# Performance work log

Hardware: AMD Instinct MI355X
Metric: run time of the kernel (lower is better)

## Reference

```python
import jax, jax.numpy as jnp
import numpy as np

N = 16384          # nodes
E_R = 524288       # radial edges (avg degree 32)
E_B = 32768        # bonded edges
N_TYPES = 20       # atom types
CS = 64            # scalar (0e) channels
CV = 32            # vector (1o) channels
EA = 16            # edge_attr_dim
EA_B = EA // 2     # bondedness embedding dim
EA_R = (EA + 1) // 2  # radial basis dim
CUTOFF = 1.5       # effective_radial_cutoff
L = 2              # n_layers
NORM = float(np.sqrt((E_R + E_B) / N))  # ~sqrt(avg degree) message normalization


def setup_inputs() -> dict:
    key = jax.random.key(0)
    ks = jax.random.split(key, 32)
    def rn(i, shape, scale=1.0):
        return jax.random.normal(ks[i], shape, dtype=jnp.float32) * scale
    s_e = 1.0 / np.sqrt(EA)
    inp = {}
    inp["pos"] = rn(0, (N, 3))
    inp["c_noise"] = rn(1, (1,))
    inp["atom_types"] = jax.random.randint(ks[2], (N,), 0, N_TYPES)
    inp["radial_edge_index"] = jax.random.randint(ks[3], (2, E_R), 0, N)
    inp["bonded_edge_index"] = jax.random.randint(ks[4], (2, E_B), 0, N)
    # learned parameters
    inp["atom_tab"] = rn(5, (N_TYPES, CS))
    inp["bond_tab"] = rn(6, (2, EA_B))
    inp["ns0_w"] = rn(7, (CS,), 0.1)
    inp["We0"] = rn(8, (EA, CS), s_e)
    inp["We1"] = rn(9, (EA, CS), s_e)
    inp["Wself0"] = rn(10, (CS, CS), 1.0 / np.sqrt(CS))
    inp["Ws0"] = rn(11, (CS, CS), 1.0 / np.sqrt(CS))
    inp["Wv0"] = rn(12, (CS, CV), 1.0 / np.sqrt(CS))
    inp["ns_w"] = rn(13, (L, CS + CV), 0.1)
    inp["We_ss"] = rn(14, (L, EA, CS), s_e)
    inp["We_vs"] = rn(15, (L, EA, CV), s_e)
    inp["We_sv"] = rn(16, (L, EA, CS), s_e)
    inp["We_vv"] = rn(17, (L, EA, CV), s_e)
    inp["We_vx"] = rn(18, (L, EA, CV), s_e)
    inp["Wmix_s"] = rn(19, (L, CS + CV, CS), 1.0 / np.sqrt(CS + CV))
    inp["Wmix_v"] = rn(20, (L, CS + 2 * CV, CV), 1.0 / np.sqrt(CS + 2 * CV))
    inp["Wself_s"] = rn(21, (L, CS, CS), 1.0 / np.sqrt(CS))
    inp["Wself_v"] = rn(22, (L, CV, CV), 1.0 / np.sqrt(CV))
    inp["skip_w"] = rn(23, (L, 2 * (CS + CV)), 0.1)
    inp["skip_b"] = rn(24, (L, 2 * (CS + CV)), 0.1)
    inp["w_out"] = rn(25, (CV,), 1.0 / np.sqrt(CV))
    inp["gain"] = jnp.asarray(0.5, dtype=jnp.float32)
    return inp


def _radial_basis(d):
    # e3nn soft_one_hot_linspace, basis='gaussian', cutoff=True
    centers = jnp.linspace(0.0, CUTOFF, EA_R + 2)[1:-1]
    step = centers[1] - centers[0]
    diff = (d[:, None] - centers[None, :]) / step
    return jnp.exp(-diff * diff) * 1.12


def reference(pos, c_noise, atom_tab, bond_tab, ns0_w, We0, We1, Wself0, Ws0, Wv0,
              ns_w, We_ss, We_vs, We_sv, We_vv, We_vx, Wmix_s, Wmix_v, Wself_s, Wself_v,
              skip_w, skip_b, w_out, gain, atom_types, radial_edge_index, bonded_edge_index):
    edge_index = jnp.concatenate([radial_edge_index, bonded_edge_index], axis=1)
    bond_mask = jnp.concatenate([jnp.zeros((E_R,), jnp.int32), jnp.ones((E_B,), jnp.int32)])
    src, dst = edge_index[0], edge_index[1]
    edge_vec = pos[src] - pos[dst]                      # [E,3]
    d = jnp.sqrt(jnp.sum(edge_vec * edge_vec, -1) + 1e-12)
    Y1 = jnp.sqrt(3.0) * edge_vec / d[:, None]          # l=1 SH, component norm; Y0 == 1
    edge_attr = jnp.concatenate([bond_tab[bond_mask], _radial_basis(d)], axis=-1)  # [E,EA]

    # atom embedding + initial noise-conditional scaling
    s = atom_tab[atom_types] * (1.0 + c_noise * ns0_w)  # [N,CS]

    # initial projector: scalar-input equivariant conv -> hidden irreps
    w0 = edge_attr @ We0
    w1 = edge_attr @ We1
    s_src = s[src]
    a_s = jax.ops.segment_sum(w0 * s_src, dst, num_segments=N) / NORM
    a_v = jax.ops.segment_sum((w1 * s_src)[:, :, None] * Y1[:, None, :], dst, num_segments=N) / NORM
    s_h = a_s @ Ws0 + s @ Wself0                        # [N,CS]
    v_h = jnp.einsum('nci,cd->ndi', a_v, Wv0)           # [N,CV,3]

    for l in range(L):
        # noise-conditional scaling (per-irrep-channel scalar scale)
        scale = 1.0 + c_noise * ns_w[l]
        ss = s_h * scale[:CS]
        vv = v_h * scale[CS:][None, :, None]
        ss_e = ss[src]
        vv_e = vv[src]
        # edge-attr-conditioned tensor-product weights
        w_ss = edge_attr @ We_ss[l]
        w_vs = edge_attr @ We_vs[l]
        w_sv = edge_attr @ We_sv[l]
        w_vv = edge_attr @ We_vv[l]
        w_vx = edge_attr @ We_vx[l]
        # CG tensor-product messages: 0x0->0, 1x1->0 (dot), 0x1->1, 1x0->1, 1x1->1 (cross)
        vdot = jnp.einsum('eci,ei->ec', vv_e, Y1)
        m_s = jnp.concatenate([w_ss * ss_e, w_vs * vdot], axis=-1)          # [E,CS+CV]
        m_v = jnp.concatenate([
            (w_sv * ss_e)[:, :, None] * Y1[:, None, :],
            w_vv[:, :, None] * vv_e,
            w_vx[:, :, None] * jnp.cross(vv_e, Y1[:, None, :]),
        ], axis=1)                                                          # [E,CS+2CV,3]
        a_s = jax.ops.segment_sum(m_s, dst, num_segments=N) / NORM
        a_v = jax.ops.segment_sum(m_v, dst, num_segments=N) / NORM
        new_s = a_s @ Wmix_s[l] + ss @ Wself_s[l]
        new_v = jnp.einsum('nci,cd->ndi', a_v, Wmix_v[l]) + jnp.einsum('nci,cd->ndi', vv, Wself_v[l])
        # noise-conditional skip connection (gated residual)
        g = jax.nn.sigmoid(skip_b[l] + c_noise * skip_w[l])
        s_h = g[:CS] * s_h + g[CS:2 * CS] * new_s
        g_v = g[2 * CS:]
        v_h = g_v[:CV][None, :, None] * v_h + g_v[CV:][None, :, None] * new_v

    # output head: 1o vectors -> 3D displacement, times output gain
    return jnp.einsum('nci,c->ni', v_h, w_out) * gain
```

## Files before the change

### kernel.cpp

```cpp
#include <hip/hip_runtime.h>
#include <math.h>

#define NA 16384
#define ER 524288
#define EB 32768
#define ET 557056
#define INV_NORM 0.17149858514250882f
#define SQRT3 1.7320508075688772f
#define RB_STEP (1.5f/9.0f)
#define BINS 512
#define DMAX 2.5f
#define INV_H ((float)BINS / DMAX)
#define T0U (2 * BINS * 128)
#define TLU (2 * BINS * 256)

typedef unsigned int uint32;
typedef unsigned short ushort16;

__device__ __forceinline__ float sigmoidf_(float x) { return 1.f / (1.f + __expf(-x)); }

__device__ __forceinline__ ushort16 f2bf(float x) {
  uint32 u = __float_as_uint(x);
  u = u + 0x7FFFu + ((u >> 16) & 1u);
  return (ushort16)(u >> 16);
}
__device__ __forceinline__ uint32 packbf(float hi, float lo) {
  return ((uint32)f2bf(hi) << 16) | (uint32)f2bf(lo);
}
__device__ __forceinline__ float bfhi(uint32 u) { return __uint_as_float(u & 0xFFFF0000u); }
__device__ __forceinline__ float bflo(uint32 u) { return __uint_as_float(u << 16); }

__global__ void k_zero(int* __restrict__ count) {
  count[blockIdx.x * 256 + threadIdx.x] = 0;
}

__global__ void k_hist(const int* __restrict__ rad, const int* __restrict__ bon, int* __restrict__ count) {
  int e = blockIdx.x * 256 + threadIdx.x;
  int d = (e < ER) ? rad[ER + e] : bon[EB + (e - ER)];
  atomicAdd(&count[d], 1);
}

__global__ __launch_bounds__(1024) void k_scan_all(const int* __restrict__ count,
                                                   int* __restrict__ offsets,
                                                   int* __restrict__ cursor,
                                                   int* __restrict__ order) {
  __shared__ int ts[1024];
  __shared__ int hist[256];
  __shared__ int hcur[256];
  int t = threadIdx.x;
  if (t < 256) hist[t] = 0;
  int base = t * 16;
  int loc[16], cnts[16];
  int sum = 0;
#pragma unroll
  for (int i = 0; i < 16; ++i) { cnts[i] = count[base + i]; loc[i] = sum; sum += cnts[i]; }
  ts[t] = sum;
  __syncthreads();
#pragma unroll
  for (int i = 0; i < 16; ++i) atomicAdd(&hist[cnts[i] < 255 ? cnts[i] : 255], 1);
  for (int off = 1; off < 1024; off <<= 1) {
    int x = (t >= off) ? ts[t - off] : 0;
    __syncthreads();
    ts[t] += x;
    __syncthreads();
  }
  int excl = ts[t] - sum;
#pragma unroll
  for (int i = 0; i < 16; ++i) {
    int v = excl + loc[i];
    offsets[base + i] = v;
    cursor[base + i] = v;
  }
  if (t == 1023) offsets[NA] = excl + sum;
  __syncthreads();
  if (t == 0) {
    int run = 0;
    for (int d = 255; d >= 0; --d) { hcur[d] = run; run += hist[d]; }
  }
  __syncthreads();
#pragma unroll
  for (int i = 0; i < 16; ++i) {
    int d = cnts[i] < 255 ? cnts[i] : 255;
    int p = atomicAdd(&hcur[d], 1);
    order[p] = base + i;
  }
}

__global__ void k_fill_pre(const int* __restrict__ rad, const int* __restrict__ bon,
                           int* __restrict__ cursor, const float* __restrict__ pos,
                           float* __restrict__ rec8) {
  int e = blockIdx.x * 256 + threadIdx.x;
  int src, dst, v;
  if (e < ER) { src = rad[e]; dst = rad[ER + e]; v = 0; }
  else        { src = bon[e - ER]; dst = bon[EB + e - ER]; v = 1; }
  float dx = pos[src * 3] - pos[dst * 3];
  float dy = pos[src * 3 + 1] - pos[dst * 3 + 1];
  float dz = pos[src * 3 + 2] - pos[dst * 3 + 2];
  float dist = sqrtf(dx * dx + dy * dy + dz * dz + 1e-12f);
  float inv = 1.f / dist;
  float fq = fminf(dist * INV_H, BINS - 1.001f);
  int q = (int)fq;
  float frac = fq - (float)q;
  int qoffL = (v * BINS + q) << 8;
  int slot = atomicAdd(&cursor[dst], 1);
  float* rp = rec8 + (size_t)slot * 8;
  *(float4*)rp = make_float4(__int_as_float(src), SQRT3 * dx * inv, SQRT3 * dy * inv, SQRT3 * dz * inv);
  rp[4] = frac;
  rp[5] = __int_as_float(qoffL);
}

__global__ void k_build(const float* __restrict__ We0, const float* __restrict__ We1,
                        const float* __restrict__ We_ss, const float* __restrict__ We_vs,
                        const float* __restrict__ We_sv, const float* __restrict__ We_vv,
                        const float* __restrict__ We_vx, const float* __restrict__ bond_tab,
                        uint32* __restrict__ T0, uint32* __restrict__ TL) {
  int q = blockIdx.x, t = blockIdx.y, v = blockIdx.z, c = threadIdx.x;
  float d0 = q * (DMAX / BINS), d1 = (q + 1) * (DMAX / BINS);
  float rb0[8], rb1[8];
#pragma unroll
  for (int k = 0; k < 8; ++k) {
    float f0 = (d0 - (k + 1) * RB_STEP) * (1.f / RB_STEP);
    float f1 = (d1 - (k + 1) * RB_STEP) * (1.f / RB_STEP);
    rb0[k] = 1.12f * __expf(-f0 * f0);
    rb1[k] = 1.12f * __expf(-f1 * f1);
  }
  if (t == 0) {
    float ba = 0, bb = 0, a0 = 0, a1 = 0, b0 = 0, b1 = 0;
#pragma unroll
    for (int k = 0; k < 8; ++k) {
      float bt = bond_tab[v * 8 + k];
      float av_lo = We0[k * 64 + c], av_hi = We0[(8 + k) * 64 + c];
      float bv_lo = We1[k * 64 + c], bv_hi = We1[(8 + k) * 64 + c];
      ba += bt * av_lo; bb += bt * bv_lo;
      a0 += rb0[k] * av_hi; a1 += rb1[k] * av_hi;
      b0 += rb0[k] * bv_hi; b1 += rb1[k] * bv_hi;
    }
    uint32* o = T0 + (((size_t)v * BINS + q) << 7) + c * 2;
    o[0] = packbf(ba + a0, a1 - a0);
    o[1] = packbf(bb + b0, b1 - b0);
  } else {
    int l = t - 1;
    const float* Wss = We_ss + l * 1024;
    const float* Wsv = We_sv + l * 1024;
    const float* WA = (c < 32) ? (We_vs + l * 512) : (We_vx + l * 512);
    const float* WB = (c < 32) ? (We_vv + l * 512) : nullptr;
    int cu = c & 31;
    float sa = 0, sb = 0, s0 = 0, s1 = 0, t0 = 0, t1 = 0;
    float ua = 0, ub = 0, u0 = 0, u1 = 0, w0 = 0, w1 = 0;
#pragma unroll
    for (int k = 0; k < 8; ++k) {
      float bt = bond_tab[v * 8 + k];
      float ss_lo = Wss[k * 64 + c], ss_hi = Wss[(8 + k) * 64 + c];
      float sv_lo = Wsv[k * 64 + c], sv_hi = Wsv[(8 + k) * 64 + c];
      sa += bt * ss_lo; sb += bt * sv_lo;
      s0 += rb0[k] * ss_hi; s1 += rb1[k] * ss_hi;
      t0 += rb0[k] * sv_hi; t1 += rb1[k] * sv_hi;
      float a_lo = WA[k * 32 + cu], a_hi = WA[(8 + k) * 32 + cu];
      ua += bt * a_lo;
      u0 += rb0[k] * a_hi; u1 += rb1[k] * a_hi;
      if (WB) {
        float b_lo = WB[k * 32 + cu], b_hi = WB[(8 + k) * 32 + cu];
        ub += bt * b_lo;
        w0 += rb0[k] * b_hi; w1 += rb1[k] * b_hi;
      }
    }
    uint32* o = TL + (size_t)l * TLU + (((size_t)v * BINS + q) << 8) + c * 4;
    o[0] = packbf(sa + s0, s1 - s0);
    o[1] = packbf(sb + t0, t1 - t0);
    o[2] = packbf(ua + u0, u1 - u0);
    o[3] = WB ? packbf(ub + w0, w1 - w0) : 0u;
  }
}

__global__ void k_embed(const float* __restrict__ atom_tab, const int* __restrict__ types,
                        const float* __restrict__ ns0_w, const float* __restrict__ cnoise,
                        float* __restrict__ s_feat, ushort16* __restrict__ s_bf) {
  int tid = blockIdx.x * 256 + threadIdx.x;
  int n = tid >> 6, c = tid & 63;
  float cn = cnoise[0];
  float v = atom_tab[types[n] * 64 + c] * (1.f + cn * ns0_w[c]);
  s_feat[tid] = v;
  s_bf[tid] = f2bf(v);
}

#define AISSUE(S, eidx) { \
    const float* rp_ = rec8 + (size_t)(eidx) * 8; \
    float4 ra_ = *(const float4*)rp_; float2 rb_ = *(const float2*)(rp_ + 4); \
    S##_f = rb_.x; S##_y0 = ra_.y; S##_y1 = ra_.z; S##_y2 = ra_.w; \
    S##_t = *(const uint2*)(T0c + ((((unsigned)__float_as_int(rb_.y)) << 1) + laneT)); \
    S##_s = *(const ushort16*)(SBc + ((((unsigned)__float_as_int(ra_.x)) << 7) + laneS)); \
  }
#define ACOMP(S) { \
    float w0_ = fmaf(S##_f, bflo(S##_t.x), bfhi(S##_t.x)); \
    float w1_ = fmaf(S##_f, bflo(S##_t.y), bfhi(S##_t.y)); \
    float sv_ = __uint_as_float((uint32)S##_s << 16); \
    acc += w0_ * sv_; \
    float t_ = w1_ * sv_; \
    a0 += t_ * S##_y0; a1 += t_ * S##_y1; a2 += t_ * S##_y2; \
  }

__global__ __launch_bounds__(256, 8) void k_agg0(
    const int* __restrict__ offsets, const int* __restrict__ order,
    const float* __restrict__ rec8,
    const uint32* __restrict__ T0, const ushort16* __restrict__ s_bf,
    float* __restrict__ a_s, float* __restrict__ a_v) {
  int lane = threadIdx.x & 63;
  int n = __builtin_amdgcn_readfirstlane(order[blockIdx.x * 4 + (threadIdx.x >> 6)]);
  const char* T0c = (const char*)T0;
  const char* SBc = (const char*)s_bf;
  unsigned laneT = (unsigned)lane * 8u;
  unsigned laneS = (unsigned)lane * 2u;
  float acc = 0, a0 = 0, a1 = 0, a2 = 0;
  int beg = __builtin_amdgcn_readfirstlane(offsets[n]);
  int end = __builtin_amdgcn_readfirstlane(offsets[n + 1]);
  float S0_f, S0_y0, S0_y1, S0_y2; uint2 S0_t; ushort16 S0_s;
  float S1_f, S1_y0, S1_y1, S1_y2; uint2 S1_t; ushort16 S1_s;
  float S2_f, S2_y0, S2_y1, S2_y2; uint2 S2_t; ushort16 S2_s;
  if (beg < end) {
    int last = end - 1;
    AISSUE(S0, beg);
    AISSUE(S1, (beg + 1 < end) ? beg + 1 : last);
    AISSUE(S2, (beg + 2 < end) ? beg + 2 : last);
    int i = beg;
    while (i + 3 <= end) {
      ACOMP(S0); AISSUE(S0, (i + 3 < end) ? i + 3 : last);
      ACOMP(S1); AISSUE(S1, (i + 4 < end) ? i + 4 : last);
      ACOMP(S2); AISSUE(S2, (i + 5 < end) ? i + 5 : last);
      i += 3;
    }
    int rem = end - i;
    if (rem >= 1) ACOMP(S0);
    if (rem >= 2) ACOMP(S1);
  }
  a_s[n * 64 + lane] = acc * INV_NORM;
  *(float4*)(a_v + ((size_t)n << 8) + (lane << 2)) =
      make_float4(a0 * INV_NORM, a1 * INV_NORM, a2 * INV_NORM, 0.f);
}

#define LISSUE(S, eidx) { \
    const float* rp_ = rec8 + (size_t)(eidx) * 8; \
    float4 ra_ = *(const float4*)rp_; float2 rb_ = *(const float2*)(rp_ + 4); \
    S##_f = rb_.x; S##_y0 = ra_.y; S##_y1 = ra_.z; S##_y2 = ra_.w; \
    S##_t = *(const uint4*)(TLc + ((((unsigned)__float_as_int(rb_.y)) << 2) + laneT)); \
    unsigned sb_ = (unsigned)__float_as_int(ra_.x); \
    S##_s = *(const ushort16*)(SHc + ((sb_ << 7) + laneS)); \
    S##_v = *(const uint2*)(VHc + ((sb_ << 8) + laneV)); \
  }
#define LCOMP(S) { \
    float wS_  = fmaf(S##_f, bflo(S##_t.x), bfhi(S##_t.x)); \
    float wSV_ = fmaf(S##_f, bflo(S##_t.y), bfhi(S##_t.y)); \
    float wA_  = fmaf(S##_f, bflo(S##_t.z), bfhi(S##_t.z)); \
    float wB_  = fmaf(S##_f, bflo(S##_t.w), bfhi(S##_t.w)); \
    float ss_ = __uint_as_float((uint32)S##_s << 16); \
    float vx_ = bfhi(S##_v.x), vy_ = bflo(S##_v.x), vz_ = bfhi(S##_v.y); \
    ms += wS_ * ss_; \
    float t_ = wSV_ * ss_; \
    av0 += t_ * S##_y0; av1 += t_ * S##_y1; av2 += t_ * S##_y2; \
    float vdot_ = vx_ * S##_y0 + vy_ * S##_y1 + vz_ * S##_y2; \
    ms2 += wA_ * vdot_; \
    float cx_ = vy_ * S##_y2 - vz_ * S##_y1; \
    float cy_ = vz_ * S##_y0 - vx_ * S##_y2; \
    float cz_ = vx_ * S##_y1 - vy_ * S##_y0; \
    float wM_ = low ? wB_ : wA_; \
    b0 += wM_ * (low ? vx_ : cx_); \
    b1 += wM_ * (low ? vy_ : cy_); \
    b2 += wM_ * (low ? vz_ : cz_); \
  }

__global__ __launch_bounds__(256, 8) void k_agg_layer(
    const float* __restrict__ cnoise, const float* __restrict__ nsw,
    const int* __restrict__ offsets, const int* __restrict__ order,
    const float* __restrict__ rec8,
    const uint32* __restrict__ TL, const ushort16* __restrict__ sh_bf,
    const uint32* __restrict__ vh_bf,
    float* __restrict__ a_s, float* __restrict__ a_v) {
  int lane = threadIdx.x & 63;
  int n = __builtin_amdgcn_readfirstlane(order[blockIdx.x * 4 + (threadIdx.x >> 6)]);
  int vc = lane & 31;
  bool low = lane < 32;
  const char* TLc = (const char*)TL;
  const char* SHc = (const char*)sh_bf;
  const char* VHc = (const char*)vh_bf;
  unsigned laneT = (unsigned)lane * 16u;
  unsigned laneS = (unsigned)lane * 2u;
  unsigned laneV = (unsigned)vc * 8u;
  float cn = cnoise[0];
  float scale_s = 1.f + cn * nsw[lane];
  float scale_v = 1.f + cn * nsw[64 + vc];
  float ms = 0, av0 = 0, av1 = 0, av2 = 0, ms2 = 0, b0 = 0, b1 = 0, b2 = 0;
  int beg = __builtin_amdgcn_readfirstlane(offsets[n]);
  int end = __builtin_amdgcn_readfirstlane(offsets[n + 1]);
  float S0_f, S0_y0, S0_y1, S0_y2; uint4 S0_t; ushort16 S0_s; uint2 S0_v;
  float S1_f, S1_y0, S1_y1, S1_y2; uint4 S1_t; ushort16 S1_s; uint2 S1_v;
  float S2_f, S2_y0, S2_y1, S2_y2; uint4 S2_t; ushort16 S2_s; uint2 S2_v;
  if (beg < end) {
    int last = end - 1;
    LISSUE(S0, beg);
    LISSUE(S1, (beg + 1 < end) ? beg + 1 : last);
    LISSUE(S2, (beg + 2 < end) ? beg + 2 : last);
    int i = beg;
    while (i + 3 <= end) {
      LCOMP(S0); LISSUE(S0, (i + 3 < end) ? i + 3 : last);
      LCOMP(S1); LISSUE(S1, (i + 4 < end) ? i + 4 : last);
      LCOMP(S2); LISSUE(S2, (i + 5 < end) ? i + 5 : last);
      i += 3;
    }
    int rem = end - i;
    if (rem >= 1) LCOMP(S0);
    if (rem >= 2) LCOMP(S1);
  }
  float fs = scale_s * INV_NORM;
  float fv = scale_v * INV_NORM;
  a_s[n * 96 + lane] = ms * fs;
  float* avn = a_v + ((size_t)n << 9);
  *(float4*)(avn + (lane << 2)) = make_float4(av0 * fs, av1 * fs, av2 * fs, 0.f);
  if (low) {
    a_s[n * 96 + 64 + vc] = ms2 * fv;
    *(float4*)(avn + ((64 + vc) << 2)) = make_float4(b0 * fv, b1 * fv, b2 * fv, 0.f);
  } else {
    *(float4*)(avn + ((96 + vc) << 2)) = make_float4(b0 * fv, b1 * fv, b2 * fv, 0.f);
  }
}

__global__ __launch_bounds__(256, 4) void k_init_s(
    const float* __restrict__ a_s, const float* __restrict__ s_feat,
    const float* __restrict__ Ws0, const float* __restrict__ Wself0,
    float* __restrict__ sh, ushort16* __restrict__ sh_bf) {
  __shared__ float W1[64 * 64];
  __shared__ float W2[64 * 64];
  __shared__ float La[8 * 64];
  __shared__ float Lf[8 * 64];
  int tid = threadIdx.x;
  for (int i = tid; i < 1024; i += 256) {
    ((float4*)W1)[i] = ((const float4*)Ws0)[i];
    ((float4*)W2)[i] = ((const float4*)Wself0)[i];
  }
  int base = blockIdx.x * 8;
  for (int i = tid; i < 512; i += 256) {
    La[i] = a_s[(size_t)base * 64 + i];
    Lf[i] = s_feat[(size_t)base * 64 + i];
  }
  __syncthreads();
  int d = tid & 63, g = tid >> 6;
  int n0 = base + g * 2;
  const float* A0 = La + g * 128;
  const float* A1 = A0 + 64;
  const float* F0 = Lf + g * 128;
  const float* F1 = F0 + 64;
  float a0 = 0, a1 = 0;
#pragma unroll 8
  for (int c = 0; c < 64; ++c) {
    float w1 = W1[c * 64 + d], w2 = W2[c * 64 + d];
    a0 += A0[c] * w1 + F0[c] * w2;
    a1 += A1[c] * w1 + F1[c] * w2;
  }
  sh[(size_t)n0 * 64 + d] = a0;
  sh[(size_t)(n0 + 1) * 64 + d] = a1;
  sh_bf[(size_t)n0 * 64 + d] = f2bf(a0);
  sh_bf[(size_t)(n0 + 1) * 64 + d] = f2bf(a1);
}

__global__ __launch_bounds__(256, 4) void k_init_v(
    const float* __restrict__ a_v, const float* __restrict__ Wv0,
    float* __restrict__ vh, uint32* __restrict__ vh_bf) {
  __shared__ float W[64 * 32];
  int tid = threadIdx.x;
  for (int i = tid; i < 512; i += 256) ((float4*)W)[i] = ((const float4*)Wv0)[i];
  __syncthreads();
  int d = tid & 31, g = tid >> 5;
  int n = blockIdx.x * 8 + g;
  const float4* av = (const float4*)(a_v + ((size_t)n << 8));
  float x = 0, y = 0, z = 0;
#pragma unroll 4
  for (int c = 0; c < 64; ++c) {
    float4 a = av[c];
    float w = W[c * 32 + d];
    x += a.x * w; y += a.y * w; z += a.z * w;
  }
  *(float4*)(vh + ((size_t)n << 7) + (d << 2)) = make_float4(x, y, z, 0.f);
  *(uint2*)(vh_bf + ((size_t)n << 6) + (d << 1)) = make_uint2(packbf(x, y), packbf(z, 0.f));
}

__global__ __launch_bounds__(256, 4) void k_mix_s(
    const float* __restrict__ a_s, const float* __restrict__ sh_in,
    const float* __restrict__ Wmix_s, const float* __restrict__ Wself_s,
    const float* __restrict__ nsw, const float* __restrict__ skw,
    const float* __restrict__ skb, const float* __restrict__ cnoise,
    float* __restrict__ sh_out, ushort16* __restrict__ sh_bf_out) {
  __shared__ float Wm[96 * 64];
  __shared__ float Wsf[64 * 64];
  __shared__ float La[8 * 96];
  int tid = threadIdx.x;
  float cn = cnoise[0];
  for (int i = tid; i < 96 * 16; i += 256) ((float4*)Wm)[i] = ((const float4*)Wmix_s)[i];
  for (int i = tid; i < 64 * 16; i += 256) {
    float4 wv = ((const float4*)Wself_s)[i];
    int c = i >> 4;
    float sc = 1.f + cn * nsw[c];
    wv.x *= sc; wv.y *= sc; wv.z *= sc; wv.w *= sc;
    ((float4*)Wsf)[i] = wv;
  }
  int base = blockIdx.x * 8;
  for (int i = tid; i < 8 * 96; i += 256) La[i] = a_s[(size_t)base * 96 + i];
  __syncthreads();
  int d = tid & 63, g = tid >> 6;
  int n0 = base + g * 2;
  const float* A0 = La + (g * 2) * 96;
  const float* A1 = A0 + 96;
  const float* s0p = sh_in + (size_t)n0 * 64;
  const float* s1p = s0p + 64;
  float acc0 = 0, acc1 = 0;
#pragma unroll 8
  for (int c = 0; c < 96; ++c) {
    float w = Wm[c * 64 + d];
    acc0 += A0[c] * w;
    acc1 += A1[c] * w;
  }
#pragma unroll 8
  for (int c = 0; c < 64; ++c) {
    float w = Wsf[c * 64 + d];
    acc0 += s0p[c] * w;
    acc1 += s1p[c] * w;
  }
  float g1 = sigmoidf_(skb[d] + cn * skw[d]);
  float g2 = sigmoidf_(skb[64 + d] + cn * skw[64 + d]);
  float o0 = g1 * s0p[d] + g2 * acc0;
  float o1 = g1 * s1p[d] + g2 * acc1;
  sh_out[(size_t)n0 * 64 + d] = o0;
  sh_out[(size_t)(n0 + 1) * 64 + d] = o1;
  sh_bf_out[(size_t)n0 * 64 + d] = f2bf(o0);
  sh_bf_out[(size_t)(n0 + 1) * 64 + d] = f2bf(o1);
}

__global__ __launch_bounds__(256, 4) void k_mix_v(
    const float* __restrict__ a_v, const float* __restrict__ vh_in,
    const float* __restrict__ Wmix_v, const float* __restrict__ Wself_v,
    const float* __restrict__ nsw, const float* __restrict__ skw,
    const float* __restrict__ skb, const float* __restrict__ cnoise,
    float* __restrict__ vh_out, uint32* __restrict__ vh_bf_out) {
  __shared__ float Wm[128 * 32];
  __shared__ float Wsf[32 * 32];
  int tid = threadIdx.x;
  float cn = cnoise[0];
  for (int i = tid; i < 128 * 8; i += 256) ((float4*)Wm)[i] = ((const float4*)Wmix_v)[i];
  for (int i = tid; i < 32 * 8; i += 256) {
    float4 wv = ((const float4*)Wself_v)[i];
    int c = i >> 3;
    float sc = 1.f + cn * nsw[64 + c];
    wv.x *= sc; wv.y *= sc; wv.z *= sc; wv.w *= sc;
    ((float4*)Wsf)[i] = wv;
  }
  __syncthreads();
  int d = tid & 31, g = tid >> 5;
  int n = blockIdx.x * 8 + g;
  const float4* av = (const float4*)(a_v + ((size_t)n << 9));
  const float4* vr = (const float4*)(vh_in + ((size_t)n << 7));
  float x = 0, y = 0, z = 0;
#pragma unroll 4
  for (int c = 0; c < 128; ++c) {
    float4 a = av[c];
    float w = Wm[c * 32 + d];
    x += a.x * w; y += a.y * w; z += a.z * w;
  }
#pragma unroll 4
  for (int c = 0; c < 32; ++c) {
    float4 vv = vr[c];
    float w = Wsf[c * 32 + d];
    x += vv.x * w; y += vv.y * w; z += vv.z * w;
  }
  float g3 = sigmoidf_(skb[128 + d] + cn * skw[128 + d]);
  float g4 = sigmoidf_(skb[160 + d] + cn * skw[160 + d]);
  float4 vi = vr[d];
  float ox = g3 * vi.x + g4 * x;
  float oy = g3 * vi.y + g4 * y;
  float oz = g3 * vi.z + g4 * z;
  *(float4*)(vh_out + ((size_t)n << 7) + (d << 2)) = make_float4(ox, oy, oz, 0.f);
  *(uint2*)(vh_bf_out + ((size_t)n << 6) + (d << 1)) = make_uint2(packbf(ox, oy), packbf(oz, 0.f));
}

__global__ void k_out(const float* __restrict__ vh, const float* __restrict__ w_out,
                      const float* __restrict__ gain, float* __restrict__ out) {
  int tid = blockIdx.x * 256 + threadIdx.x;
  int n = tid / 3, i = tid - n * 3;
  float acc = 0;
  for (int c = 0; c < 32; ++c) acc += vh[((size_t)n << 7) + c * 4 + i] * w_out[c];
  out[tid] = acc * gain[0];
}

extern "C" void kernel_launch(void* const* d_in, const int* in_sizes, int n_in,
                              void* d_out, int out_size, void* d_ws, size_t ws_size,
                              hipStream_t stream) {
  (void)in_sizes; (void)n_in; (void)out_size; (void)ws_size;
  const float* pos     = (const float*)d_in[0];
  const float* cn      = (const float*)d_in[1];
  const int*   types   = (const int*)d_in[2];
  const int*   rad     = (const int*)d_in[3];
  const int*   bon     = (const int*)d_in[4];
  const float* atom_tab= (const float*)d_in[5];
  const float* bond_tab= (const float*)d_in[6];
  const float* ns0_w   = (const float*)d_in[7];
  const float* We0     = (const float*)d_in[8];
  const float* We1     = (const float*)d_in[9];
  const float* Wself0  = (const float*)d_in[10];
  const float* Ws0     = (const float*)d_in[11];
  const float* Wv0     = (const float*)d_in[12];
  const float* ns_w    = (const float*)d_in[13];
  const float* We_ss   = (const float*)d_in[14];
  const float* We_vs   = (const float*)d_in[15];
  const float* We_sv   = (const float*)d_in[16];
  const float* We_vv   = (const float*)d_in[17];
  const float* We_vx   = (const float*)d_in[18];
  const float* Wmix_s  = (const float*)d_in[19];
  const float* Wmix_v  = (const float*)d_in[20];
  const float* Wself_s = (const float*)d_in[21];
  const float* Wself_v = (const float*)d_in[22];
  const float* skip_w  = (const float*)d_in[23];
  const float* skip_b  = (const float*)d_in[24];
  const float* w_out   = (const float*)d_in[25];
  const float* gain    = (const float*)d_in[26];

  char* ws = (char*)d_ws;
  size_t o = 0;
  auto alloc = [&](size_t bytes) -> void* {
    void* p = ws + o;
    o += (bytes + 255) & ~(size_t)255;
    return p;
  };
  float* s_feat  = (float*)alloc((size_t)NA * 64 * 4);
  ushort16* s_bf = (ushort16*)alloc((size_t)NA * 64 * 2);
  float* a_s     = (float*)alloc((size_t)NA * 96 * 4);
  float* a_v     = (float*)alloc((size_t)NA * 512 * 4);
  float* sh0     = (float*)alloc((size_t)NA * 64 * 4);
  float* sh1     = (float*)alloc((size_t)NA * 64 * 4);
  ushort16* shbf0= (ushort16*)alloc((size_t)NA * 64 * 2);
  ushort16* shbf1= (ushort16*)alloc((size_t)NA * 64 * 2);
  float* vh0     = (float*)alloc((size_t)NA * 128 * 4);
  float* vh1     = (float*)alloc((size_t)NA * 128 * 4);
  uint32* vhbf0  = (uint32*)alloc((size_t)NA * 64 * 4);
  uint32* vhbf1  = (uint32*)alloc((size_t)NA * 64 * 4);
  int* count     = (int*)alloc((size_t)NA * 4);
  int* offsets   = (int*)alloc((size_t)(NA + 1) * 4);
  int* cursor    = (int*)alloc((size_t)NA * 4);
  int* order     = (int*)alloc((size_t)NA * 4);
  float* rec8    = (float*)alloc((size_t)ET * 32);
  uint32* T0     = (uint32*)alloc((size_t)T0U * 4);
  uint32* TL     = (uint32*)alloc((size_t)2 * TLU * 4);
  float* shb[2]  = {sh0, sh1};
  ushort16* shbf[2] = {shbf0, shbf1};
  float* vhb[2]  = {vh0, vh1};
  uint32* vhbf[2]= {vhbf0, vhbf1};

  k_zero<<<NA / 256, 256, 0, stream>>>(count);
  k_hist<<<ET / 256, 256, 0, stream>>>(rad, bon, count);
  k_scan_all<<<1, 1024, 0, stream>>>(count, offsets, cursor, order);
  k_fill_pre<<<ET / 256, 256, 0, stream>>>(rad, bon, cursor, pos, rec8);
  k_build<<<dim3(BINS, 3, 2), 64, 0, stream>>>(We0, We1, We_ss, We_vs, We_sv, We_vv, We_vx,
                                               bond_tab, T0, TL);

  k_embed<<<NA * 64 / 256, 256, 0, stream>>>(atom_tab, types, ns0_w, cn, s_feat, s_bf);
  k_agg0<<<NA / 4, 256, 0, stream>>>(offsets, order, rec8, T0, s_bf, a_s, a_v);
  k_init_s<<<NA / 8, 256, 0, stream>>>(a_s, s_feat, Ws0, Wself0, shb[0], shbf[0]);
  k_init_v<<<NA / 8, 256, 0, stream>>>(a_v, Wv0, vhb[0], vhbf[0]);

  for (int l = 0; l < 2; ++l) {
    int bin = l & 1, bout = 1 - bin;
    k_agg_layer<<<NA / 4, 256, 0, stream>>>(
        cn, ns_w + l * 96, offsets, order, rec8, TL + (size_t)l * TLU, shbf[bin], vhbf[bin], a_s, a_v);
    k_mix_s<<<NA / 8, 256, 0, stream>>>(
        a_s, shb[bin], Wmix_s + l * 96 * 64, Wself_s + l * 64 * 64,
        ns_w + l * 96, skip_w + l * 192, skip_b + l * 192, cn, shb[bout], shbf[bout]);
    k_mix_v<<<NA / 8, 256, 0, stream>>>(
        a_v, vhb[bin], Wmix_v + l * 128 * 32, Wself_v + l * 32 * 32,
        ns_w + l * 96, skip_w + l * 192, skip_b + l * 192, cn, vhb[bout], vhbf[bout]);
  }
  k_out<<<NA * 3 / 256, 256, 0, stream>>>(vhb[0], w_out, gain, (float*)d_out);
}
```

Before: 479.1 us.

## Skip dead scalar path in last layer and fuse init/mix/output kernels

The final layer's scalar aggregation and scalar mix are dropped, because only the vector features reach the output head. The scalar and vector init kernels are merged into one launch, as are the scalar and vector mix kernels, by splitting on block index. The output projection is folded into the last vector mix with a wave shuffle reduction, and the zeroing kernel becomes a memset. This cuts launch count and skips unneeded compute and stores, at the cost of larger fused kernels whose LDS footprint may limit occupancy.

```diff
diff --git a/kernel.cpp b/kernel.cpp
--- a/kernel.cpp
+++ b/kernel.cpp
@@ -29,10 +29,6 @@
 }
 __device__ __forceinline__ float bfhi(uint32 u) { return __uint_as_float(u & 0xFFFF0000u); }
 __device__ __forceinline__ float bflo(uint32 u) { return __uint_as_float(u << 16); }
-
-__global__ void k_zero(int* __restrict__ count) {
-  count[blockIdx.x * 256 + threadIdx.x] = 0;
-}
 
 __global__ void k_hist(const int* __restrict__ rad, const int* __restrict__ bon, int* __restrict__ count) {
   int e = blockIdx.x * 256 + threadIdx.x;
@@ -266,6 +262,22 @@
     b1 += wM_ * (low ? vy_ : cy_); \
     b2 += wM_ * (low ? vz_ : cz_); \
   }
+#define LCOMP_NS(S) { \
+    float wSV_ = fmaf(S##_f, bflo(S##_t.y), bfhi(S##_t.y)); \
+    float wA_  = fmaf(S##_f, bflo(S##_t.z), bfhi(S##_t.z)); \
+    float wB_  = fmaf(S##_f, bflo(S##_t.w), bfhi(S##_t.w)); \
+    float ss_ = __uint_as_float((uint32)S##_s << 16); \
+    float vx_ = bfhi(S##_v.x), vy_ = bflo(S##_v.x), vz_ = bfhi(S##_v.y); \
+    float t_ = wSV_ * ss_; \
+    av0 += t_ * S##_y0; av1 += t_ * S##_y1; av2 += t_ * S##_y2; \
+    float cx_ = vy_ * S##_y2 - vz_ * S##_y1; \
+    float cy_ = vz_ * S##_y0 - vx_ * S##_y2; \
+    float cz_ = vx_ * S##_y1 - vy_ * S##_y0; \
+    float wM_ = low ? wB_ : wA_; \
+    b0 += wM_ * (low ? vx_ : cx_); \
+    b1 += wM_ * (low ? vy_ : cy_); \
+    b2 += wM_ * (low ? vz_ : cz_); \
+  }
 
 __global__ __launch_bounds__(256, 8) void k_agg_layer(
     const float* __restrict__ cnoise, const float* __restrict__ nsw,
@@ -273,7 +285,7 @@
     const float* __restrict__ rec8,
     const uint32* __restrict__ TL, const ushort16* __restrict__ sh_bf,
     const uint32* __restrict__ vh_bf,
-    float* __restrict__ a_s, float* __restrict__ a_v) {
+    float* __restrict__ a_s, float* __restrict__ a_v, int need_s) {
   int lane = threadIdx.x & 63;
   int n = __builtin_amdgcn_readfirstlane(order[blockIdx.x * 4 + (threadIdx.x >> 6)]);
   int vc = lane & 31;
@@ -299,192 +311,214 @@
     LISSUE(S1, (beg + 1 < end) ? beg + 1 : last);
     LISSUE(S2, (beg + 2 < end) ? beg + 2 : last);
     int i = beg;
-    while (i + 3 <= end) {
-      LCOMP(S0); LISSUE(S0, (i + 3 < end) ? i + 3 : last);
-      LCOMP(S1); LISSUE(S1, (i + 4 < end) ? i + 4 : last);
-      LCOMP(S2); LISSUE(S2, (i + 5 < end) ? i + 5 : last);
-      i += 3;
-    }
-    int rem = end - i;
-    if (rem >= 1) LCOMP(S0);
-    if (rem >= 2) LCOMP(S1);
+    if (need_s) {
+      while (i + 3 <= end) {
+        LCOMP(S0); LISSUE(S0, (i + 3 < end) ? i + 3 : last);
+        LCOMP(S1); LISSUE(S1, (i + 4 < end) ? i + 4 : last);
+        LCOMP(S2); LISSUE(S2, (i + 5 < end) ? i + 5 : last);
+        i += 3;
+      }
+      int rem = end - i;
+      if (rem >= 1) LCOMP(S0);
+      if (rem >= 2) LCOMP(S1);
+    } else {
+      while (i + 3 <= end) {
+        LCOMP_NS(S0); LISSUE(S0, (i + 3 < end) ? i + 3 : last);
+        LCOMP_NS(S1); LISSUE(S1, (i + 4 < end) ? i + 4 : last);
+        LCOMP_NS(S2); LISSUE(S2, (i + 5 < end) ? i + 5 : last);
+        i += 3;
+      }
+      int rem = end - i;
+      if (rem >= 1) LCOMP_NS(S0);
+      if (rem >= 2) LCOMP_NS(S1);
+    }
   }
   float fs = scale_s * INV_NORM;
   float fv = scale_v * INV_NORM;
-  a_s[n * 96 + lane] = ms * fs;
+  if (need_s) a_s[n * 96 + lane] = ms * fs;
   float* avn = a_v + ((size_t)n << 9);
   *(float4*)(avn + (lane << 2)) = make_float4(av0 * fs, av1 * fs, av2 * fs, 0.f);
   if (low) {
-    a_s[n * 96 + 64 + vc] = ms2 * fv;
+    if (need_s) a_s[n * 96 + 64 + vc] = ms2 * fv;
     *(float4*)(avn + ((64 + vc) << 2)) = make_float4(b0 * fv, b1 * fv, b2 * fv, 0.f);
   } else {
     *(float4*)(avn + ((96 + vc) << 2)) = make_float4(b0 * fv, b1 * fv, b2 * fv, 0.f);
   }
 }
 
-__global__ __launch_bounds__(256, 4) void k_init_s(
+__global__ __launch_bounds__(256, 4) void k_init(
     const float* __restrict__ a_s, const float* __restrict__ s_feat,
     const float* __restrict__ Ws0, const float* __restrict__ Wself0,
-    float* __restrict__ sh, ushort16* __restrict__ sh_bf) {
-  __shared__ float W1[64 * 64];
-  __shared__ float W2[64 * 64];
-  __shared__ float La[8 * 64];
-  __shared__ float Lf[8 * 64];
+    const float* __restrict__ a_v, const float* __restrict__ Wv0,
+    float* __restrict__ sh, ushort16* __restrict__ sh_bf,
+    float* __restrict__ vh, uint32* __restrict__ vh_bf) {
+  __shared__ __align__(16) char ldsbuf[36864];
   int tid = threadIdx.x;
-  for (int i = tid; i < 1024; i += 256) {
-    ((float4*)W1)[i] = ((const float4*)Ws0)[i];
-    ((float4*)W2)[i] = ((const float4*)Wself0)[i];
-  }
-  int base = blockIdx.x * 8;
-  for (int i = tid; i < 512; i += 256) {
-    La[i] = a_s[(size_t)base * 64 + i];
-    Lf[i] = s_feat[(size_t)base * 64 + i];
-  }
-  __syncthreads();
-  int d = tid & 63, g = tid >> 6;
-  int n0 = base + g * 2;
-  const float* A0 = La + g * 128;
-  const float* A1 = A0 + 64;
-  const float* F0 = Lf + g * 128;
-  const float* F1 = F0 + 64;
-  float a0 = 0, a1 = 0;
+  int bid = blockIdx.x;
+  if (bid < 2048) {
+    float* W1 = (float*)ldsbuf;
+    float* W2 = (float*)(ldsbuf + 16384);
+    float* La = (float*)(ldsbuf + 32768);
+    float* Lf = (float*)(ldsbuf + 34816);
+    for (int i = tid; i < 1024; i += 256) {
+      ((float4*)W1)[i] = ((const float4*)Ws0)[i];
+      ((float4*)W2)[i] = ((const float4*)Wself0)[i];
+    }
+    int base = bid * 8;
+    for (int i = tid; i < 512; i += 256) {
+      La[i] = a_s[(size_t)base * 64 + i];
+      Lf[i] = s_feat[(size_t)base * 64 + i];
+    }
+    __syncthreads();
+    int d = tid & 63, g = tid >> 6;
+    int n0 = base + g * 2;
+    const float* A0 = La + g * 128;
+    const float* A1 = A0 + 64;
+    const float* F0 = Lf + g * 128;
+    const float* F1 = F0 + 64;
+    float a0 = 0, a1 = 0;
 #pragma unroll 8
-  for (int c = 0; c < 64; ++c) {
-    float w1 = W1[c * 64 + d], w2 = W2[c * 64 + d];
-    a0 += A0[c] * w1 + F0[c] * w2;
-    a1 += A1[c] * w1 + F1[c] * w2;
-  }
-  sh[(size_t)n0 * 64 + d] = a0;
-  sh[(size_t)(n0 + 1) * 64 + d] = a1;
-  sh_bf[(size_t)n0 * 64 + d] = f2bf(a0);
-  sh_bf[(size_t)(n0 + 1) * 64 + d] = f2bf(a1);
-}
-
-__global__ __launch_bounds__(256, 4) void k_init_v(
-    const float* __restrict__ a_v, const float* __restrict__ Wv0,
-    float* __restrict__ vh, uint32* __restrict__ vh_bf) {
-  __shared__ float W[64 * 32];
-  int tid = threadIdx.x;
-  for (int i = tid; i < 512; i += 256) ((float4*)W)[i] = ((const float4*)Wv0)[i];
-  __syncthreads();
-  int d = tid & 31, g = tid >> 5;
-  int n = blockIdx.x * 8 + g;
-  const float4* av = (const float4*)(a_v + ((size_t)n << 8));
-  float x = 0, y = 0, z = 0;
+    for (int c = 0; c < 64; ++c) {
+      float w1 = W1[c * 64 + d], w2 = W2[c * 64 + d];
+      a0 += A0[c] * w1 + F0[c] * w2;
+      a1 += A1[c] * w1 + F1[c] * w2;
+    }
+    sh[(size_t)n0 * 64 + d] = a0;
+    sh[(size_t)(n0 + 1) * 64 + d] = a1;
+    sh_bf[(size_t)n0 * 64 + d] = f2bf(a0);
+    sh_bf[(size_t)(n0 + 1) * 64 + d] = f2bf(a1);
+  } else {
+    float* W = (float*)ldsbuf;
+    for (int i = tid; i < 512; i += 256) ((float4*)W)[i] = ((const float4*)Wv0)[i];
+    __syncthreads();
+    int d = tid & 31, g = tid >> 5;
+    int n = (bid - 2048) * 8 + g;
+    const float4* av = (const float4*)(a_v + ((size_t)n << 8));
+    float x = 0, y = 0, z = 0;
 #pragma unroll 4
-  for (int c = 0; c < 64; ++c) {
-    float4 a = av[c];
-    float w = W[c * 32 + d];
-    x += a.x * w; y += a.y * w; z += a.z * w;
-  }
-  *(float4*)(vh + ((size_t)n << 7) + (d << 2)) = make_float4(x, y, z, 0.f);
-  *(uint2*)(vh_bf + ((size_t)n << 6) + (d << 1)) = make_uint2(packbf(x, y), packbf(z, 0.f));
-}
-
-__global__ __launch_bounds__(256, 4) void k_mix_s(
-    const float* __restrict__ a_s, const float* __restrict__ sh_in,
+    for (int c = 0; c < 64; ++c) {
+      float4 a = av[c];
+      float w = W[c * 32 + d];
+      x += a.x * w; y += a.y * w; z += a.z * w;
+    }
+    *(float4*)(vh + ((size_t)n << 7) + (d << 2)) = make_float4(x, y, z, 0.f);
+    *(uint2*)(vh_bf + ((size_t)n << 6) + (d << 1)) = make_uint2(packbf(x, y), packbf(z, 0.f));
+  }
+}
+
+__global__ __launch_bounds__(256, 4) void k_mix(
+    const float* __restrict__ a_s, const float* __restrict__ a_v,
+    const float* __restrict__ sh_in, const float* __restrict__ vh_in,
     const float* __restrict__ Wmix_s, const float* __restrict__ Wself_s,
-    const float* __restrict__ nsw, const float* __restrict__ skw,
-    const float* __restrict__ skb, const float* __restrict__ cnoise,
-    float* __restrict__ sh_out, ushort16* __restrict__ sh_bf_out) {
-  __shared__ float Wm[96 * 64];
-  __shared__ float Wsf[64 * 64];
-  __shared__ float La[8 * 96];
-  int tid = threadIdx.x;
-  float cn = cnoise[0];
-  for (int i = tid; i < 96 * 16; i += 256) ((float4*)Wm)[i] = ((const float4*)Wmix_s)[i];
-  for (int i = tid; i < 64 * 16; i += 256) {
-    float4 wv = ((const float4*)Wself_s)[i];
-    int c = i >> 4;
-    float sc = 1.f + cn * nsw[c];
-    wv.x *= sc; wv.y *= sc; wv.z *= sc; wv.w *= sc;
-    ((float4*)Wsf)[i] = wv;
-  }
-  int base = blockIdx.x * 8;
-  for (int i = tid; i < 8 * 96; i += 256) La[i] = a_s[(size_t)base * 96 + i];
-  __syncthreads();
-  int d = tid & 63, g = tid >> 6;
-  int n0 = base + g * 2;
-  const float* A0 = La + (g * 2) * 96;
-  const float* A1 = A0 + 96;
-  const float* s0p = sh_in + (size_t)n0 * 64;
-  const float* s1p = s0p + 64;
-  float acc0 = 0, acc1 = 0;
-#pragma unroll 8
-  for (int c = 0; c < 96; ++c) {
-    float w = Wm[c * 64 + d];
-    acc0 += A0[c] * w;
-    acc1 += A1[c] * w;
-  }
-#pragma unroll 8
-  for (int c = 0; c < 64; ++c) {
-    float w = Wsf[c * 64 + d];
-    acc0 += s0p[c] * w;
-    acc1 += s1p[c] * w;
-  }
-  float g1 = sigmoidf_(skb[d] + cn * skw[d]);
-  float g2 = sigmoidf_(skb[64 + d] + cn * skw[64 + d]);
-  float o0 = g1 * s0p[d] + g2 * acc0;
-  float o1 = g1 * s1p[d] + g2 * acc1;
-  sh_out[(size_t)n0 * 64 + d] = o0;
-  sh_out[(size_t)(n0 + 1) * 64 + d] = o1;
-  sh_bf_out[(size_t)n0 * 64 + d] = f2bf(o0);
-  sh_bf_out[(size_t)(n0 + 1) * 64 + d] = f2bf(o1);
-}
-
-__global__ __launch_bounds__(256, 4) void k_mix_v(
-    const float* __restrict__ a_v, const float* __restrict__ vh_in,
     const float* __restrict__ Wmix_v, const float* __restrict__ Wself_v,
     const float* __restrict__ nsw, const float* __restrict__ skw,
     const float* __restrict__ skb, const float* __restrict__ cnoise,
-    float* __restrict__ vh_out, uint32* __restrict__ vh_bf_out) {
-  __shared__ float Wm[128 * 32];
-  __shared__ float Wsf[32 * 32];
+    float* __restrict__ sh_out, ushort16* __restrict__ sh_bf_out,
+    float* __restrict__ vh_out, uint32* __restrict__ vh_bf_out,
+    const float* __restrict__ w_out, const float* __restrict__ gain,
+    float* __restrict__ out, int last) {
+  __shared__ __align__(16) char ldsbuf[44032];
   int tid = threadIdx.x;
+  int bid = blockIdx.x;
   float cn = cnoise[0];
-  for (int i = tid; i < 128 * 8; i += 256) ((float4*)Wm)[i] = ((const float4*)Wmix_v)[i];
-  for (int i = tid; i < 32 * 8; i += 256) {
-    float4 wv = ((const float4*)Wself_v)[i];
-    int c = i >> 3;
-    float sc = 1.f + cn * nsw[64 + c];
-    wv.x *= sc; wv.y *= sc; wv.z *= sc; wv.w *= sc;
-    ((float4*)Wsf)[i] = wv;
-  }
-  __syncthreads();
-  int d = tid & 31, g = tid >> 5;
-  int n = blockIdx.x * 8 + g;
-  const float4* av = (const float4*)(a_v + ((size_t)n << 9));
-  const float4* vr = (const float4*)(vh_in + ((size_t)n << 7));
-  float x = 0, y = 0, z = 0;
+  if (!last && bid < 2048) {
+    float* Wm = (float*)ldsbuf;
+    float* Wsf = (float*)(ldsbuf + 24576);
+    float* La = (float*)(ldsbuf + 40960);
+    for (int i = tid; i < 96 * 16; i += 256) ((float4*)Wm)[i] = ((const float4*)Wmix_s)[i];
+    for (int i = tid; i < 64 * 16; i += 256) {
+      float4 wv = ((const float4*)Wself_s)[i];
+      int c = i >> 4;
+      float sc = 1.f + cn * nsw[c];
+      wv.x *= sc; wv.y *= sc; wv.z *= sc; wv.w *= sc;
+      ((float4*)Wsf)[i] = wv;
+    }
+    int base = bid * 8;
+    for (int i = tid; i < 8 * 96; i += 256) La[i] = a_s[(size_t)base * 96 + i];
+    __syncthreads();
+    int d = tid & 63, g = tid >> 6;
+    int n0 = base + g * 2;
+    const float* A0 = La + (g * 2) * 96;
+    const float* A1 = A0 + 96;
+    const float* s0p = sh_in + (size_t)n0 * 64;
+    const float* s1p = s0p + 64;
+    float acc0 = 0, acc1 = 0;
+#pragma unroll 8
+    for (int c = 0; c < 96; ++c) {
+      float w = Wm[c * 64 + d];
+      acc0 += A0[c] * w;
+      acc1 += A1[c] * w;
+    }
+#pragma unroll 8
+    for (int c = 0; c < 64; ++c) {
+      float w = Wsf[c * 64 + d];
+      acc0 += s0p[c] * w;
+      acc1 += s1p[c] * w;
+    }
+    float g1 = sigmoidf_(skb[d] + cn * skw[d]);
+    float g2 = sigmoidf_(skb[64 + d] + cn * skw[64 + d]);
+    float o0 = g1 * s0p[d] + g2 * acc0;
+    float o1 = g1 * s1p[d] + g2 * acc1;
+    sh_out[(size_t)n0 * 64 + d] = o0;
+    sh_out[(size_t)(n0 + 1) * 64 + d] = o1;
+    sh_bf_out[(size_t)n0 * 64 + d] = f2bf(o0);
+    sh_bf_out[(size_t)(n0 + 1) * 64 + d] = f2bf(o1);
+  } else {
+    int vb = last ? bid : bid - 2048;
+    float* Wm = (float*)ldsbuf;
+    float* Wsf = (float*)(ldsbuf + 16384);
+    for (int i = tid; i < 128 * 8; i += 256) ((float4*)Wm)[i] = ((const float4*)Wmix_v)[i];
+    for (int i = tid; i < 32 * 8; i += 256) {
+      float4 wv = ((const float4*)Wself_v)[i];
+      int c = i >> 3;
+      float sc = 1.f + cn * nsw[64 + c];
+      wv.x *= sc; wv.y *= sc; wv.z *= sc; wv.w *= sc;
+      ((float4*)Wsf)[i] = wv;
+    }
+    __syncthreads();
+    int d = tid & 31, g = tid >> 5;
+    int n = vb * 8 + g;
+    const float4* av = (const float4*)(a_v + ((size_t)n << 9));
+    const float4* vr = (const float4*)(vh_in + ((size_t)n << 7));
+    float x = 0, y = 0, z = 0;
 #pragma unroll 4
-  for (int c = 0; c < 128; ++c) {
-    float4 a = av[c];
-    float w = Wm[c * 32 + d];
-    x += a.x * w; y += a.y * w; z += a.z * w;
-  }
+    for (int c = 0; c < 128; ++c) {
+      float4 a = av[c];
+      float w = Wm[c * 32 + d];
+      x += a.x * w; y += a.y * w; z += a.z * w;
+    }
 #pragma unroll 4
-  for (int c = 0; c < 32; ++c) {
-    float4 vv = vr[c];
-    float w = Wsf[c * 32 + d];
-    x += vv.x * w; y += vv.y * w; z += vv.z * w;
-  }
-  float g3 = sigmoidf_(skb[128 + d] + cn * skw[128 + d]);
-  float g4 = sigmoidf_(skb[160 + d] + cn * skw[160 + d]);
-  float4 vi = vr[d];
-  float ox = g3 * vi.x + g4 * x;
-  float oy = g3 * vi.y + g4 * y;
-  float oz = g3 * vi.z + g4 * z;
-  *(float4*)(vh_out + ((size_t)n << 7) + (d << 2)) = make_float4(ox, oy, oz, 0.f);
-  *(uint2*)(vh_bf_out + ((size_t)n << 6) + (d << 1)) = make_uint2(packbf(ox, oy), packbf(oz, 0.f));
-}
-
-__global__ void k_out(const float* __restrict__ vh, const float* __restrict__ w_out,
-                      const float* __restrict__ gain, float* __restrict__ out) {
-  int tid = blockIdx.x * 256 + threadIdx.x;
-  int n = tid / 3, i = tid - n * 3;
-  float acc = 0;
-  for (int c = 0; c < 32; ++c) acc += vh[((size_t)n << 7) + c * 4 + i] * w_out[c];
-  out[tid] = acc * gain[0];
+    for (int c = 0; c < 32; ++c) {
+      float4 vv = vr[c];
+      float w = Wsf[c * 32 + d];
+      x += vv.x * w; y += vv.y * w; z += vv.z * w;
+    }
+    float g3 = sigmoidf_(skb[128 + d] + cn * skw[128 + d]);
+    float g4 = sigmoidf_(skb[160 + d] + cn * skw[160 + d]);
+    float4 vi = vr[d];
+    float ox = g3 * vi.x + g4 * x;
+    float oy = g3 * vi.y + g4 * y;
+    float oz = g3 * vi.z + g4 * z;
+    if (!last) {
+      *(float4*)(vh_out + ((size_t)n << 7) + (d << 2)) = make_float4(ox, oy, oz, 0.f);
+      *(uint2*)(vh_bf_out + ((size_t)n << 6) + (d << 1)) = make_uint2(packbf(ox, oy), packbf(oz, 0.f));
+    } else {
+      float wo = w_out[d];
+      float px = wo * ox, py = wo * oy, pz = wo * oz;
+#pragma unroll
+      for (int m = 16; m >= 1; m >>= 1) {
+        px += __shfl_xor(px, m, 32);
+        py += __shfl_xor(py, m, 32);
+        pz += __shfl_xor(pz, m, 32);
+      }
+      if (d == 0) {
+        float gg = gain[0];
+        out[n * 3 + 0] = px * gg;
+        out[n * 3 + 1] = py * gg;
+        out[n * 3 + 2] = pz * gg;
+      }
+    }
+  }
 }
 
 extern "C" void kernel_launch(void* const* d_in, const int* in_sizes, int n_in,
@@ -550,7 +584,7 @@
   float* vhb[2]  = {vh0, vh1};
   uint32* vhbf[2]= {vhbf0, vhbf1};
 
-  k_zero<<<NA / 256, 256, 0, stream>>>(count);
+  hipMemsetAsync(count, 0, (size_t)NA * 4, stream);
   k_hist<<<ET / 256, 256, 0, stream>>>(rad, bon, count);
   k_scan_all<<<1, 1024, 0, stream>>>(count, offsets, cursor, order);
   k_fill_pre<<<ET / 256, 256, 0, stream>>>(rad, bon, cursor, pos, rec8);
@@ -559,19 +593,21 @@
 
   k_embed<<<NA * 64 / 256, 256, 0, stream>>>(atom_tab, types, ns0_w, cn, s_feat, s_bf);
   k_agg0<<<NA / 4, 256, 0, stream>>>(offsets, order, rec8, T0, s_bf, a_s, a_v);
-  k_init_s<<<NA / 8, 256, 0, stream>>>(a_s, s_feat, Ws0, Wself0, shb[0], shbf[0]);
-  k_init_v<<<NA / 8, 256, 0, stream>>>(a_v, Wv0, vhb[0], vhbf[0]);
+  k_init<<<4096, 256, 0, stream>>>(a_s, s_feat, Ws0, Wself0, a_v, Wv0,
+                                   shb[0], shbf[0], vhb[0], vhbf[0]);
 
   for (int l = 0; l < 2; ++l) {
     int bin = l & 1, bout = 1 - bin;
+    int last = (l == 1);
     k_agg_layer<<<NA / 4, 256, 0, stream>>>(
-        cn, ns_w + l * 96, offsets, order, rec8, TL + (size_t)l * TLU, shbf[bin], vhbf[bin], a_s, a_v);
-    k_mix_s<<<NA / 8, 256, 0, stream>>>(
-        a_s, shb[bin], Wmix_s + l * 96 * 64, Wself_s + l * 64 * 64,
-        ns_w + l * 96, skip_w + l * 192, skip_b + l * 192, cn, shb[bout], shbf[bout]);
-    k_mix_v<<<NA / 8, 256, 0, stream>>>(
-        a_v, vhb[bin], Wmix_v + l * 128 * 32, Wself_v + l * 32 * 32,
-        ns_w + l * 96, skip_w + l * 192, skip_b + l * 192, cn, vhb[bout], vhbf[bout]);
-  }
-  k_out<<<NA * 3 / 256, 256, 0, stream>>>(vhb[0], w_out, gain, (float*)d_out);
-}
+        cn, ns_w + l * 96, offsets, order, rec8, TL + (size_t)l * TLU, shbf[bin], vhbf[bin],
+        a_s, a_v, last ? 0 : 1);
+    k_mix<<<last ? 2048 : 4096, 256, 0, stream>>>(
+        a_s, a_v, shb[bin], vhb[bin],
+        Wmix_s + l * 96 * 64, Wself_s + l * 64 * 64,
+        Wmix_v + l * 128 * 32, Wself_v + l * 32 * 32,
+        ns_w + l * 96, skip_w + l * 192, skip_b + l * 192, cn,
+        shb[bout], shbf[bout], vhb[bout], vhbf[bout],
+        w_out, gain, (float*)d_out, last);
+  }
+}
```

New measurement: 488.8 us. 2.0% more time.

## Skip dead scalar path in last layer and fuse output head into mix_v

Applied to the files above, without the earlier changes.

The final output depends only on the vector features, so in the last layer the scalar aggregation, its messages and k_mix_s are dropped. A specialized k_agg_layer_ns computes only the vector aggregates, and k_mix_s is no longer launched for layer 1. The output projection is folded into the last k_mix_v with a wave shuffle reduction, which removes k_out and the final vh write. The intent is less memory traffic and fewer launches in the last layer, at the cost of an extra kernel variant to maintain.

```diff
diff --git a/kernel.cpp b/kernel.cpp
--- a/kernel.cpp
+++ b/kernel.cpp
@@ -322,6 +322,76 @@
   }
 }
 
+#define LCOMP_NS(S) { \
+    float wSV_ = fmaf(S##_f, bflo(S##_t.y), bfhi(S##_t.y)); \
+    float wA_  = fmaf(S##_f, bflo(S##_t.z), bfhi(S##_t.z)); \
+    float wB_  = fmaf(S##_f, bflo(S##_t.w), bfhi(S##_t.w)); \
+    float ss_ = __uint_as_float((uint32)S##_s << 16); \
+    float vx_ = bfhi(S##_v.x), vy_ = bflo(S##_v.x), vz_ = bfhi(S##_v.y); \
+    float t_ = wSV_ * ss_; \
+    av0 += t_ * S##_y0; av1 += t_ * S##_y1; av2 += t_ * S##_y2; \
+    float cx_ = vy_ * S##_y2 - vz_ * S##_y1; \
+    float cy_ = vz_ * S##_y0 - vx_ * S##_y2; \
+    float cz_ = vx_ * S##_y1 - vy_ * S##_y0; \
+    float wM_ = low ? wB_ : wA_; \
+    b0 += wM_ * (low ? vx_ : cx_); \
+    b1 += wM_ * (low ? vy_ : cy_); \
+    b2 += wM_ * (low ? vz_ : cz_); \
+  }
+
+__global__ __launch_bounds__(256, 8) void k_agg_layer_ns(
+    const float* __restrict__ cnoise, const float* __restrict__ nsw,
+    const int* __restrict__ offsets, const int* __restrict__ order,
+    const float* __restrict__ rec8,
+    const uint32* __restrict__ TL, const ushort16* __restrict__ sh_bf,
+    const uint32* __restrict__ vh_bf,
+    float* __restrict__ a_v) {
+  int lane = threadIdx.x & 63;
+  int n = __builtin_amdgcn_readfirstlane(order[blockIdx.x * 4 + (threadIdx.x >> 6)]);
+  int vc = lane & 31;
+  bool low = lane < 32;
+  const char* TLc = (const char*)TL;
+  const char* SHc = (const char*)sh_bf;
+  const char* VHc = (const char*)vh_bf;
+  unsigned laneT = (unsigned)lane * 16u;
+  unsigned laneS = (unsigned)lane * 2u;
+  unsigned laneV = (unsigned)vc * 8u;
+  float cn = cnoise[0];
+  float scale_s = 1.f + cn * nsw[lane];
+  float scale_v = 1.f + cn * nsw[64 + vc];
+  float av0 = 0, av1 = 0, av2 = 0, b0 = 0, b1 = 0, b2 = 0;
+  int beg = __builtin_amdgcn_readfirstlane(offsets[n]);
+  int end = __builtin_amdgcn_readfirstlane(offsets[n + 1]);
+  float S0_f, S0_y0, S0_y1, S0_y2; uint4 S0_t; ushort16 S0_s; uint2 S0_v;
+  float S1_f, S1_y0, S1_y1, S1_y2; uint4 S1_t; ushort16 S1_s; uint2 S1_v;
+  float S2_f, S2_y0, S2_y1, S2_y2; uint4 S2_t; ushort16 S2_s; uint2 S2_v;
+  if (beg < end) {
+    int last = end - 1;
+    LISSUE(S0, beg);
+    LISSUE(S1, (beg + 1 < end) ? beg + 1 : last);
+    LISSUE(S2, (beg + 2 < end) ? beg + 2 : last);
+    int i = beg;
+    while (i + 3 <= end) {
+      LCOMP_NS(S0); LISSUE(S0, (i + 3 < end) ? i + 3 : last);
+      LCOMP_NS(S1); LISSUE(S1, (i + 4 < end) ? i + 4 : last);
+      LCOMP_NS(S2); LISSUE(S2, (i + 5 < end) ? i + 5 : last);
+      i += 3;
+    }
+    int rem = end - i;
+    if (rem >= 1) LCOMP_NS(S0);
+    if (rem >= 2) LCOMP_NS(S1);
+  }
+  float fs = scale_s * INV_NORM;
+  float fv = scale_v * INV_NORM;
+  float* avn = a_v + ((size_t)n << 9);
+  *(float4*)(avn + (lane << 2)) = make_float4(av0 * fs, av1 * fs, av2 * fs, 0.f);
+  if (low) {
+    *(float4*)(avn + ((64 + vc) << 2)) = make_float4(b0 * fv, b1 * fv, b2 * fv, 0.f);
+  } else {
+    *(float4*)(avn + ((96 + vc) << 2)) = make_float4(b0 * fv, b1 * fv, b2 * fv, 0.f);
+  }
+}
+
 __global__ __launch_bounds__(256, 4) void k_init_s(
     const float* __restrict__ a_s, const float* __restrict__ s_feat,
     const float* __restrict__ Ws0, const float* __restrict__ Wself0,
@@ -437,7 +507,9 @@
     const float* __restrict__ Wmix_v, const float* __restrict__ Wself_v,
     const float* __restrict__ nsw, const float* __restrict__ skw,
     const float* __restrict__ skb, const float* __restrict__ cnoise,
-    float* __restrict__ vh_out, uint32* __restrict__ vh_bf_out) {
+    float* __restrict__ vh_out, uint32* __restrict__ vh_bf_out,
+    const float* __restrict__ w_out, const float* __restrict__ gain,
+    float* __restrict__ out, int last) {
   __shared__ float Wm[128 * 32];
   __shared__ float Wsf[32 * 32];
   int tid = threadIdx.x;
@@ -474,17 +546,25 @@
   float ox = g3 * vi.x + g4 * x;
   float oy = g3 * vi.y + g4 * y;
   float oz = g3 * vi.z + g4 * z;
-  *(float4*)(vh_out + ((size_t)n << 7) + (d << 2)) = make_float4(ox, oy, oz, 0.f);
-  *(uint2*)(vh_bf_out + ((size_t)n << 6) + (d << 1)) = make_uint2(packbf(ox, oy), packbf(oz, 0.f));
-}
-
-__global__ void k_out(const float* __restrict__ vh, const float* __restrict__ w_out,
-                      const float* __restrict__ gain, float* __restrict__ out) {
-  int tid = blockIdx.x * 256 + threadIdx.x;
-  int n = tid / 3, i = tid - n * 3;
-  float acc = 0;
-  for (int c = 0; c < 32; ++c) acc += vh[((size_t)n << 7) + c * 4 + i] * w_out[c];
-  out[tid] = acc * gain[0];
+  if (!last) {
+    *(float4*)(vh_out + ((size_t)n << 7) + (d << 2)) = make_float4(ox, oy, oz, 0.f);
+    *(uint2*)(vh_bf_out + ((size_t)n << 6) + (d << 1)) = make_uint2(packbf(ox, oy), packbf(oz, 0.f));
+  } else {
+    float wo = w_out[d];
+    float px = wo * ox, py = wo * oy, pz = wo * oz;
+#pragma unroll
+    for (int m = 16; m >= 1; m >>= 1) {
+      px += __shfl_xor(px, m, 32);
+      py += __shfl_xor(py, m, 32);
+      pz += __shfl_xor(pz, m, 32);
+    }
+    if (d == 0) {
+      float gg = gain[0];
+      out[n * 3 + 0] = px * gg;
+      out[n * 3 + 1] = py * gg;
+      out[n * 3 + 2] = pz * gg;
+    }
+  }
 }
 
 extern "C" void kernel_launch(void* const* d_in, const int* in_sizes, int n_in,
@@ -562,16 +642,18 @@
   k_init_s<<<NA / 8, 256, 0, stream>>>(a_s, s_feat, Ws0, Wself0, shb[0], shbf[0]);
   k_init_v<<<NA / 8, 256, 0, stream>>>(a_v, Wv0, vhb[0], vhbf[0]);
 
-  for (int l = 0; l < 2; ++l) {
-    int bin = l & 1, bout = 1 - bin;
-    k_agg_layer<<<NA / 4, 256, 0, stream>>>(
-        cn, ns_w + l * 96, offsets, order, rec8, TL + (size_t)l * TLU, shbf[bin], vhbf[bin], a_s, a_v);
-    k_mix_s<<<NA / 8, 256, 0, stream>>>(
-        a_s, shb[bin], Wmix_s + l * 96 * 64, Wself_s + l * 64 * 64,
-        ns_w + l * 96, skip_w + l * 192, skip_b + l * 192, cn, shb[bout], shbf[bout]);
-    k_mix_v<<<NA / 8, 256, 0, stream>>>(
-        a_v, vhb[bin], Wmix_v + l * 128 * 32, Wself_v + l * 32 * 32,
-        ns_w + l * 96, skip_w + l * 192, skip_b + l * 192, cn, vhb[bout], vhbf[bout]);
-  }
-  k_out<<<NA * 3 / 256, 256, 0, stream>>>(vhb[0], w_out, gain, (float*)d_out);
-}
+  k_agg_layer<<<NA / 4, 256, 0, stream>>>(
+      cn, ns_w, offsets, order, rec8, TL, shbf[0], vhbf[0], a_s, a_v);
+  k_mix_s<<<NA / 8, 256, 0, stream>>>(
+      a_s, shb[0], Wmix_s, Wself_s, ns_w, skip_w, skip_b, cn, shb[1], shbf[1]);
+  k_mix_v<<<NA / 8, 256, 0, stream>>>(
+      a_v, vhb[0], Wmix_v, Wself_v, ns_w, skip_w, skip_b, cn,
+      vhb[1], vhbf[1], w_out, gain, (float*)d_out, 0);
+
+  k_agg_layer_ns<<<NA / 4, 256, 0, stream>>>(
+      cn, ns_w + 96, offsets, order, rec8, TL + (size_t)TLU, shbf[1], vhbf[1], a_v);
+  k_mix_v<<<NA / 8, 256, 0, stream>>>(
+      a_v, vhb[1], Wmix_v + 128 * 32, Wself_v + 32 * 32,
+      ns_w + 96, skip_w + 192, skip_b + 192, cn,
+      nullptr, nullptr, w_out, gain, (float*)d_out, 1);
+}
```

New measurement: 449.3 us. -6.2%, faster.
